# Optimization experiments

Measured on AMD Instinct MI355X. Metric: run time of the kernel, lower is better.

Reference implementation:

```python
import jax, jax.numpy as jnp
import numpy as np

N_HEAD = 4
N_FEAT = 256
D_K = N_FEAT // N_HEAD


def setup_inputs() -> dict:
    key = jax.random.key(0)
    ks = jax.random.split(key, 7)
    B, T, F = 8, 2048, N_FEAT
    return {
        "query": jax.random.normal(ks[0], (B, T, F), dtype=jnp.float32),
        "key": jax.random.normal(ks[1], (B, T, F), dtype=jnp.float32),
        "value": jax.random.normal(ks[2], (B, T, F), dtype=jnp.float32),
        "mask": jax.random.randint(ks[3], (B, 1, T), 0, 2, dtype=jnp.int32),
        "W_qkv": jax.random.normal(ks[4], (3 * F, 3 * F), dtype=jnp.float32) * 0.02,
        "b_qkv": jnp.zeros((3 * F,), dtype=jnp.float32),
        "W_out": jax.random.normal(ks[5], (F, F), dtype=jnp.float32) * 0.02,
        "b_out": jnp.zeros((F,), dtype=jnp.float32),
    }


def reference(query, key, value, mask, W_qkv, b_qkv, W_out, b_out):
    B, T, F = query.shape
    H, dk = N_HEAD, D_K
    # fused QKV projection on concatenated [q; k; v]  -> (B, T, 3F)
    qkv = jnp.concatenate([query, key, value], axis=-1) @ W_qkv.T + b_qkv
    qkv = qkv.reshape(B, T, H, 3 * dk)
    q, k, v = jnp.split(qkv, 3, axis=-1)          # each (B, T, H, dk)
    q = q.transpose(0, 2, 1, 3)                    # (B, H, T, dk)
    k = k.transpose(0, 2, 1, 3)
    v = v.transpose(0, 2, 1, 3)
    scores = jnp.einsum("bhqd,bhkd->bhqk", q, k) / jnp.sqrt(jnp.float32(dk))
    # mask: (B, 1, T) -> broadcast (B, 1, 1, T); positions where mask==0 are masked
    m = (mask[:, None, :, :] == 0)
    min_val = jnp.finfo(scores.dtype).min
    scores = jnp.where(m, min_val, scores)
    attn = jax.nn.softmax(scores, axis=-1)
    attn = jnp.where(m, jnp.float32(0.0), attn)    # zero masked probs, as in torch code
    x = jnp.einsum("bhqk,bhkd->bhqd", attn, v)     # (B, H, T, dk)
    x = x.transpose(0, 2, 1, 3).reshape(B, T, H * dk)
    return x @ W_out.T + b_out
```

## Files before the change

### kernel.cpp

```cpp
#include <hip/hip_runtime.h>
#include <hip/hip_bf16.h>

#define NB 8
#define NT 2048
#define NH 4
#define NF 256
#define NTF 768
#define NM (NB * NT)

typedef unsigned short u16;
typedef unsigned long long u64;
typedef u16 u16x8 __attribute__((ext_vector_type(8)));
typedef __bf16 bf16x8 __attribute__((ext_vector_type(8)));
typedef float f32x4 __attribute__((ext_vector_type(4)));

__device__ __forceinline__ u16 bf16_rne(float f) {
    union { float f; unsigned u; } x; x.f = f;
    unsigned u = x.u;
    return (u16)((u + 0x7fffu + ((u >> 16) & 1u)) >> 16);
}

__device__ __forceinline__ int swz(int row, int colB) {
    return row * 128 + (colB ^ ((row & 7) << 4));
}

__device__ __forceinline__ void glds16(const void* g, void* l) {
    __builtin_amdgcn_global_load_lds(
        (const __attribute__((address_space(1))) void*)g,
        (__attribute__((address_space(3))) void*)l, 16, 0, 0);
}
__device__ __forceinline__ void glds4(const void* g, void* l) {
    __builtin_amdgcn_global_load_lds(
        (const __attribute__((address_space(1))) void*)g,
        (__attribute__((address_space(3))) void*)l, 4, 0, 0);
}

__global__ __launch_bounds__(256) void convert_all_kernel(
        const float* __restrict__ q, const float* __restrict__ k,
        const float* __restrict__ v, const float* __restrict__ wqkv,
        const float* __restrict__ wout, const int* __restrict__ mask,
        u16* __restrict__ xcat, u16* __restrict__ wqkvb,
        u16* __restrict__ woutb, float* __restrict__ maskadd) {
    int bid = blockIdx.x;
    if (bid < 6144) {
        int tid = bid * 256 + threadIdx.x;
        int row = tid / 96;
        int c8  = (tid % 96) * 8;
        const float* src; int c;
        if (c8 < NF)            { src = q; c = c8; }
        else if (c8 < 2 * NF)   { src = k; c = c8 - NF; }
        else                    { src = v; c = c8 - 2 * NF; }
        const float4* p = reinterpret_cast<const float4*>(src + (size_t)row * NF + c);
        float4 a = p[0], b = p[1];
        u16x8 o;
        o[0] = bf16_rne(a.x); o[1] = bf16_rne(a.y); o[2] = bf16_rne(a.z); o[3] = bf16_rne(a.w);
        o[4] = bf16_rne(b.x); o[5] = bf16_rne(b.y); o[6] = bf16_rne(b.z); o[7] = bf16_rne(b.w);
        *reinterpret_cast<u16x8*>(xcat + (size_t)row * NTF + c8) = o;
    } else if (bid < 6464) {
        int tid = (bid - 6144) * 256 + threadIdx.x;
        int i8 = tid * 8;
        const float* src; u16* dst; int off;
        if (i8 < NTF * NTF) { src = wqkv; dst = wqkvb; off = i8; }
        else                { src = wout; dst = woutb; off = i8 - NTF * NTF; }
        const float4* p = reinterpret_cast<const float4*>(src + off);
        float4 a = p[0], b = p[1];
        u16x8 o;
        o[0] = bf16_rne(a.x); o[1] = bf16_rne(a.y); o[2] = bf16_rne(a.z); o[3] = bf16_rne(a.w);
        o[4] = bf16_rne(b.x); o[5] = bf16_rne(b.y); o[6] = bf16_rne(b.z); o[7] = bf16_rne(b.w);
        *reinterpret_cast<u16x8*>(dst + off) = o;
    } else {
        int i = (bid - 6464) * 2048 + threadIdx.x * 8;
        int4 m0 = *reinterpret_cast<const int4*>(mask + i);
        int4 m1 = *reinterpret_cast<const int4*>(mask + i + 4);
        float4 f0 = { m0.x ? 0.f : -1e30f, m0.y ? 0.f : -1e30f,
                      m0.z ? 0.f : -1e30f, m0.w ? 0.f : -1e30f };
        float4 f1 = { m1.x ? 0.f : -1e30f, m1.y ? 0.f : -1e30f,
                      m1.z ? 0.f : -1e30f, m1.w ? 0.f : -1e30f };
        *reinterpret_cast<float4*>(maskadd + i) = f0;
        *reinterpret_cast<float4*>(maskadd + i + 4) = f1;
    }
}

template<int N, int K, int MODE>
__global__ __launch_bounds__(256) void gemm_kernel(
        const u16* __restrict__ A, const u16* __restrict__ Bw,
        const float* __restrict__ bias, void* __restrict__ Cout,
        u16* __restrict__ Vt) {
    __shared__ alignas(16) char smem[32768];
    char* As = smem;
    char* Bs = smem + 16384;
    int m0 = blockIdx.x * 64, n0 = blockIdx.y * 64;
    int tid = threadIdx.x;
    int w = tid >> 6, lane = tid & 63, l15 = lane & 15, hi = lane >> 4;
    int r0 = tid >> 3, cb0 = (tid & 7) * 16;
    int gcb = cb0 ^ ((r0 & 7) << 4);
    int wo = w * 1024;

    const char* Ac = (const char*)A;
    const char* Bc = (const char*)Bw;
    const char* ga0 = Ac + (size_t)(m0 + r0) * (K * 2) + gcb;
    const char* ga1 = ga0 + (size_t)32 * (K * 2);
    const char* gb0 = Bc + (size_t)(n0 + r0) * (K * 2) + gcb;
    const char* gb1 = gb0 + (size_t)32 * (K * 2);

    glds16(ga0, As + wo); glds16(ga1, As + 4096 + wo);
    glds16(gb0, Bs + wo); glds16(gb1, Bs + 4096 + wo);

    f32x4 acc[4];
#pragma unroll
    for (int ct = 0; ct < 4; ++ct) acc[ct] = (f32x4){0.f, 0.f, 0.f, 0.f};

    constexpr int NKT = K / 64;
    for (int kt = 0; kt < NKT; ++kt) {
        int cur = kt & 1;
        __syncthreads();
        if (kt + 1 < NKT) {
            int off = (kt + 1) * 128;
            char* Ad = As + (cur ^ 1) * 8192;
            char* Bd = Bs + (cur ^ 1) * 8192;
            glds16(ga0 + off, Ad + wo); glds16(ga1 + off, Ad + 4096 + wo);
            glds16(gb0 + off, Bd + wo); glds16(gb1 + off, Bd + 4096 + wo);
        }
        const char* Ax = As + cur * 8192;
        const char* Bx = Bs + cur * 8192;
#pragma unroll
        for (int ks = 0; ks < 2; ++ks) {
            bf16x8 af = *reinterpret_cast<const bf16x8*>(Ax + swz(w * 16 + l15, hi * 16 + ks * 64));
#pragma unroll
            for (int ct = 0; ct < 4; ++ct) {
                bf16x8 bf = *reinterpret_cast<const bf16x8*>(Bx + swz(ct * 16 + l15, hi * 16 + ks * 64));
                acc[ct] = __builtin_amdgcn_mfma_f32_16x16x32_bf16(af, bf, acc[ct], 0, 0, 0);
            }
        }
    }

    int orow = m0 + w * 16 + hi * 4;
    if (MODE == 2 && ((n0 >> 6) % 3) == 2) {
        int b = orow >> 11, t = orow & (NT - 1);
        int bh = b * NH + (n0 / 192);
#pragma unroll
        for (int ct = 0; ct < 4; ++ct) {
            int d = ct * 16 + l15;
            float bv = bias[n0 + d];
            union { u16 h4[4]; u64 u; } pk;
#pragma unroll
            for (int r = 0; r < 4; ++r) pk.h4[r] = bf16_rne(acc[ct][r] + bv);
            *reinterpret_cast<u64*>(Vt + (size_t)(bh * 64 + d) * NT + t) = pk.u;
        }
    } else {
#pragma unroll
        for (int ct = 0; ct < 4; ++ct) {
            int col = n0 + ct * 16 + l15;
            float bv = bias[col];
#pragma unroll
            for (int r = 0; r < 4; ++r) {
                float val = acc[ct][r] + bv;
                if (MODE == 1)
                    reinterpret_cast<float*>(Cout)[(size_t)(orow + r) * N + col] = val;
                else
                    reinterpret_cast<u16*>(Cout)[(size_t)(orow + r) * N + col] = bf16_rne(val);
            }
        }
    }
}

__global__ __launch_bounds__(512) void attn_kernel(
        const u16* __restrict__ qkv, const u16* __restrict__ vt,
        const float* __restrict__ maskadd, u16* __restrict__ xout) {
    int bh = blockIdx.x;
    int q0 = blockIdx.y * 128;
    int b = bh >> 2, h = bh & 3;
    __shared__ alignas(16) char smem[49664];
    char* Ps = smem + 32768;
    int tid = threadIdx.x;
    int w = tid >> 6, lane = tid & 63, l15 = lane & 15, hi = lane >> 4;
    int r0 = tid >> 3, cb0 = (tid & 7) * 16;
    int gcb = cb0 ^ ((r0 & 7) << 4);
    int wo = w * 1024;
    const float SCALE = 0.125f * 1.44269504088896340736f;

    const char* qkvC = (const char*)qkv;
    const char* vtC  = (const char*)vt;
    const char* gq0 = qkvC + (size_t)(b * NT + q0 + r0) * 1536 + h * 384 + gcb;
    const char* gq1 = gq0 + (size_t)64 * 1536;
    const char* gk0 = qkvC + (size_t)(b * NT + r0) * 1536 + h * 384 + 128 + gcb;
    const char* gv0 = vtC + (size_t)(bh * 64 + r0) * (NT * 2) + gcb;
    const char* gm  = (const char*)maskadd + (size_t)(b * NT + lane) * 4;

    glds16(gq0, Ps + wo);           glds16(gq1, Ps + 8192 + wo);
    glds16(gk0, smem + wo);
    glds16(gv0, smem + 16384 + wo);
    if (w == 0) glds4(gm, smem + 49152);

    f32x4 accO[4];
#pragma unroll
    for (int ct = 0; ct < 4; ++ct) accO[ct] = (f32x4){0.f, 0.f, 0.f, 0.f};
    float ssum = 0.f;
    bf16x8 bQ[2];
    char* Pw = Ps + w * 2048;

    for (int kt = 0; kt < NT / 64; ++kt) {
        int cur = kt & 1;
        __syncthreads();
        if (kt == 0) {
#pragma unroll
            for (int ks = 0; ks < 2; ++ks)
                bQ[ks] = *reinterpret_cast<const bf16x8*>(Ps + swz(w * 16 + l15, hi * 16 + ks * 64));
        }
        if (kt < NT / 64 - 1) {
            char* Kd = smem + (cur ^ 1) * 8192;
            char* Vd = smem + 16384 + (cur ^ 1) * 8192;
            glds16(gk0 + (size_t)(kt + 1) * 98304, Kd + wo);
            glds16(gv0 + (kt + 1) * 128, Vd + wo);
            if (w == 0) glds4(gm + (kt + 1) * 256, smem + 49152 + (cur ^ 1) * 256);
        }
        const char* Kx = smem + cur * 8192;
        const char* Vx = smem + 16384 + cur * 8192;
        const float* mF = reinterpret_cast<const float*>(smem + 49152 + cur * 256);

        f32x4 s[4];
#pragma unroll
        for (int ct = 0; ct < 4; ++ct) s[ct] = (f32x4){0.f, 0.f, 0.f, 0.f};
        __builtin_amdgcn_s_setprio(1);
#pragma unroll
        for (int ks = 0; ks < 2; ++ks) {
#pragma unroll
            for (int ct = 0; ct < 4; ++ct) {
                bf16x8 aK = *reinterpret_cast<const bf16x8*>(Kx + swz(ct * 16 + l15, hi * 16 + ks * 64));
                s[ct] = __builtin_amdgcn_mfma_f32_16x16x32_bf16(aK, bQ[ks], s[ct], 0, 0, 0);
            }
        }
        __builtin_amdgcn_s_setprio(0);
        float rs = 0.f;
#pragma unroll
        for (int ct = 0; ct < 4; ++ct) {
            f32x4 madd = *reinterpret_cast<const f32x4*>(mF + ct * 16 + hi * 4);
#pragma unroll
            for (int r = 0; r < 4; ++r) {
                float p = exp2f(__builtin_fmaf(s[ct][r], SCALE, madd[r]));
                s[ct][r] = p;
                rs += p;
            }
        }
        ssum += rs;
#pragma unroll
        for (int ct = 0; ct < 4; ++ct) {
            union { __bf16 h4[4]; u64 u; } pk;
#pragma unroll
            for (int r = 0; r < 4; ++r) pk.h4[r] = (__bf16)s[ct][r];
            *reinterpret_cast<u64*>(Pw + swz(l15, ct * 32 + hi * 8)) = pk.u;
        }
        bf16x8 aP[2];
#pragma unroll
        for (int ks = 0; ks < 2; ++ks)
            aP[ks] = *reinterpret_cast<const bf16x8*>(Pw + swz(l15, hi * 16 + ks * 64));
        __builtin_amdgcn_s_setprio(1);
#pragma unroll
        for (int ks = 0; ks < 2; ++ks)
#pragma unroll
            for (int ct = 0; ct < 4; ++ct) {
                bf16x8 bV = *reinterpret_cast<const bf16x8*>(Vx + swz(ct * 16 + l15, hi * 16 + ks * 64));
                accO[ct] = __builtin_amdgcn_mfma_f32_16x16x32_bf16(aP[ks], bV, accO[ct], 0, 0, 0);
            }
        __builtin_amdgcn_s_setprio(0);
    }
    ssum += __shfl_xor(ssum, 16, 64);
    ssum += __shfl_xor(ssum, 32, 64);
    __syncthreads();
    float* sS = reinterpret_cast<float*>(smem + 49152);
    if (hi == 0) sS[w * 16 + l15] = ssum;
    f32x4 sq = *reinterpret_cast<const f32x4*>(sS + w * 16 + hi * 4);
    int qrow = q0 + w * 16 + hi * 4;
#pragma unroll
    for (int r = 0; r < 4; ++r) {
        float inv = sq[r] > 0.f ? 1.0f / sq[r] : 0.0f;
#pragma unroll
        for (int ct = 0; ct < 4; ++ct) {
            int d = ct * 16 + l15;
            xout[(size_t)(b * NT + qrow + r) * NF + h * 64 + d] = bf16_rne(accO[ct][r] * inv);
        }
    }
}

extern "C" void kernel_launch(void* const* d_in, const int* in_sizes, int n_in,
                              void* d_out, int out_size, void* d_ws, size_t ws_size,
                              hipStream_t stream) {
    const float* q    = (const float*)d_in[0];
    const float* k    = (const float*)d_in[1];
    const float* v    = (const float*)d_in[2];
    const int*   mask = (const int*)d_in[3];
    const float* wqkv = (const float*)d_in[4];
    const float* bqkv = (const float*)d_in[5];
    const float* wout = (const float*)d_in[6];
    const float* bout = (const float*)d_in[7];
    float* out = (float*)d_out;

    char* ws = (char*)d_ws;
    u16*   Xcat    = (u16*)(ws);
    u16*   QKV     = (u16*)(ws + 25165824);
    u16*   Vt      = (u16*)(ws + 50331648);
    u16*   Xattn   = (u16*)(ws + 58720256);
    u16*   Wqkvb   = (u16*)(ws + 67108864);
    u16*   Woutb   = (u16*)(ws + 68288512);
    float* Maskadd = (float*)(ws + 68419584);

    convert_all_kernel<<<6472, 256, 0, stream>>>(q, k, v, wqkv, wout, mask,
                                                 Xcat, Wqkvb, Woutb, Maskadd);
    gemm_kernel<NTF, NTF, 2><<<dim3(NM / 64, NTF / 64), 256, 0, stream>>>(
        Xcat, Wqkvb, bqkv, QKV, Vt);
    attn_kernel<<<dim3(NB * NH, NT / 128), 512, 0, stream>>>(QKV, Vt, Maskadd, Xattn);
    gemm_kernel<NF, NF, 1><<<dim3(NM / 64, NF / 64), 256, 0, stream>>>(
        Xattn, Woutb, bout, out, nullptr);
}
```

Baseline: 115.9 us.

## Software-pipeline attention loop: defer PV MFMA by one tile, read mask from global

Restructures the attention inner loop so that the P·V multiply for tile kt-1 runs after the QK^T and softmax of tile kt, with double-buffered P in LDS. V loads are issued one iteration later than K loads so they have a full iteration to land. The mask is now read straight from global memory instead of being staged in LDS. The aim is to overlap exp work with MFMA and drop LDS traffic, at the cost of 64KB of LDS per block, which may lower occupancy.

```diff
diff --git a/kernel.cpp b/kernel.cpp
--- a/kernel.cpp
+++ b/kernel.cpp
@@ -28,11 +28,6 @@
     __builtin_amdgcn_global_load_lds(
         (const __attribute__((address_space(1))) void*)g,
         (__attribute__((address_space(3))) void*)l, 16, 0, 0);
-}
-__device__ __forceinline__ void glds4(const void* g, void* l) {
-    __builtin_amdgcn_global_load_lds(
-        (const __attribute__((address_space(1))) void*)g,
-        (__attribute__((address_space(3))) void*)l, 4, 0, 0);
 }
 
 __global__ __launch_bounds__(256) void convert_all_kernel(
@@ -170,8 +165,10 @@
     int bh = blockIdx.x;
     int q0 = blockIdx.y * 128;
     int b = bh >> 2, h = bh & 3;
-    __shared__ alignas(16) char smem[49664];
-    char* Ps = smem + 32768;
+    __shared__ alignas(16) char smem[65536];
+    char* Kb = smem;
+    char* Vb = smem + 16384;
+    char* Pb = smem + 32768;
     int tid = threadIdx.x;
     int w = tid >> 6, lane = tid & 63, l15 = lane & 15, hi = lane >> 4;
     int r0 = tid >> 3, cb0 = (tid & 7) * 16;
@@ -185,19 +182,17 @@
     const char* gq1 = gq0 + (size_t)64 * 1536;
     const char* gk0 = qkvC + (size_t)(b * NT + r0) * 1536 + h * 384 + 128 + gcb;
     const char* gv0 = vtC + (size_t)(bh * 64 + r0) * (NT * 2) + gcb;
-    const char* gm  = (const char*)maskadd + (size_t)(b * NT + lane) * 4;
-
-    glds16(gq0, Ps + wo);           glds16(gq1, Ps + 8192 + wo);
-    glds16(gk0, smem + wo);
-    glds16(gv0, smem + 16384 + wo);
-    if (w == 0) glds4(gm, smem + 49152);
+    const float* gm = maskadd + (size_t)b * NT;
+
+    glds16(gq0, Pb + 16384 + wo);
+    glds16(gq1, Pb + 16384 + 8192 + wo);
+    glds16(gk0, Kb + wo);
 
     f32x4 accO[4];
 #pragma unroll
     for (int ct = 0; ct < 4; ++ct) accO[ct] = (f32x4){0.f, 0.f, 0.f, 0.f};
     float ssum = 0.f;
     bf16x8 bQ[2];
-    char* Pw = Ps + w * 2048;
 
     for (int kt = 0; kt < NT / 64; ++kt) {
         int cur = kt & 1;
@@ -205,19 +200,14 @@
         if (kt == 0) {
 #pragma unroll
             for (int ks = 0; ks < 2; ++ks)
-                bQ[ks] = *reinterpret_cast<const bf16x8*>(Ps + swz(w * 16 + l15, hi * 16 + ks * 64));
-        }
-        if (kt < NT / 64 - 1) {
-            char* Kd = smem + (cur ^ 1) * 8192;
-            char* Vd = smem + 16384 + (cur ^ 1) * 8192;
-            glds16(gk0 + (size_t)(kt + 1) * 98304, Kd + wo);
-            glds16(gv0 + (kt + 1) * 128, Vd + wo);
-            if (w == 0) glds4(gm + (kt + 1) * 256, smem + 49152 + (cur ^ 1) * 256);
-        }
-        const char* Kx = smem + cur * 8192;
-        const char* Vx = smem + 16384 + cur * 8192;
-        const float* mF = reinterpret_cast<const float*>(smem + 49152 + cur * 256);
-
+                bQ[ks] = *reinterpret_cast<const bf16x8*>(
+                    Pb + 16384 + swz(w * 16 + l15, hi * 16 + ks * 64));
+        }
+        if (kt < NT / 64 - 1)
+            glds16(gk0 + (size_t)(kt + 1) * 98304, Kb + (cur ^ 1) * 8192 + wo);
+        glds16(gv0 + kt * 128, Vb + cur * 8192 + wo);
+
+        const char* Kx = Kb + cur * 8192;
         f32x4 s[4];
 #pragma unroll
         for (int ct = 0; ct < 4; ++ct) s[ct] = (f32x4){0.f, 0.f, 0.f, 0.f};
@@ -231,18 +221,22 @@
             }
         }
         __builtin_amdgcn_s_setprio(0);
+
+        const float4* mrow = reinterpret_cast<const float4*>(gm + kt * 64);
         float rs = 0.f;
 #pragma unroll
         for (int ct = 0; ct < 4; ++ct) {
-            f32x4 madd = *reinterpret_cast<const f32x4*>(mF + ct * 16 + hi * 4);
+            float4 madd = mrow[ct * 4 + hi];
+            float m4[4] = {madd.x, madd.y, madd.z, madd.w};
 #pragma unroll
             for (int r = 0; r < 4; ++r) {
-                float p = exp2f(__builtin_fmaf(s[ct][r], SCALE, madd[r]));
+                float p = exp2f(__builtin_fmaf(s[ct][r], SCALE, m4[r]));
                 s[ct][r] = p;
                 rs += p;
             }
         }
         ssum += rs;
+        char* Pw = Pb + cur * 16384 + w * 2048;
 #pragma unroll
         for (int ct = 0; ct < 4; ++ct) {
             union { __bf16 h4[4]; u64 u; } pk;
@@ -250,11 +244,34 @@
             for (int r = 0; r < 4; ++r) pk.h4[r] = (__bf16)s[ct][r];
             *reinterpret_cast<u64*>(Pw + swz(l15, ct * 32 + hi * 8)) = pk.u;
         }
+
+        if (kt > 0) {
+            char* Pprev = Pb + (cur ^ 1) * 16384 + w * 2048;
+            const char* Vx = Vb + (cur ^ 1) * 8192;
+            bf16x8 aP[2];
+#pragma unroll
+            for (int ks = 0; ks < 2; ++ks)
+                aP[ks] = *reinterpret_cast<const bf16x8*>(Pprev + swz(l15, hi * 16 + ks * 64));
+            __builtin_amdgcn_s_setprio(1);
+#pragma unroll
+            for (int ks = 0; ks < 2; ++ks)
+#pragma unroll
+                for (int ct = 0; ct < 4; ++ct) {
+                    bf16x8 bV = *reinterpret_cast<const bf16x8*>(Vx + swz(ct * 16 + l15, hi * 16 + ks * 64));
+                    accO[ct] = __builtin_amdgcn_mfma_f32_16x16x32_bf16(aP[ks], bV, accO[ct], 0, 0, 0);
+                }
+            __builtin_amdgcn_s_setprio(0);
+        }
+    }
+
+    __syncthreads();
+    {
+        char* Pprev = Pb + 16384 + w * 2048;
+        const char* Vx = Vb + 8192;
         bf16x8 aP[2];
 #pragma unroll
         for (int ks = 0; ks < 2; ++ks)
-            aP[ks] = *reinterpret_cast<const bf16x8*>(Pw + swz(l15, hi * 16 + ks * 64));
-        __builtin_amdgcn_s_setprio(1);
+            aP[ks] = *reinterpret_cast<const bf16x8*>(Pprev + swz(l15, hi * 16 + ks * 64));
 #pragma unroll
         for (int ks = 0; ks < 2; ++ks)
 #pragma unroll
@@ -262,14 +279,12 @@
                 bf16x8 bV = *reinterpret_cast<const bf16x8*>(Vx + swz(ct * 16 + l15, hi * 16 + ks * 64));
                 accO[ct] = __builtin_amdgcn_mfma_f32_16x16x32_bf16(aP[ks], bV, accO[ct], 0, 0, 0);
             }
-        __builtin_amdgcn_s_setprio(0);
     }
     ssum += __shfl_xor(ssum, 16, 64);
     ssum += __shfl_xor(ssum, 32, 64);
-    __syncthreads();
-    float* sS = reinterpret_cast<float*>(smem + 49152);
-    if (hi == 0) sS[w * 16 + l15] = ssum;
-    f32x4 sq = *reinterpret_cast<const f32x4*>(sS + w * 16 + hi * 4);
+    float* sS = reinterpret_cast<float*>(Pb) + w * 16;
+    if (hi == 0) sS[l15] = ssum;
+    f32x4 sq = *reinterpret_cast<const f32x4*>(sS + hi * 4);
     int qrow = q0 + w * 16 + hi * 4;
 #pragma unroll
     for (int r = 0; r < 4; ++r) {
```

Measured after the change: 115.7 us. No clear change (-0.2%).

## Rewrite attention with 32x32 MFMA, register-resident P and split-K warp groups

Applied to the files above, without the earlier changes.

Rewrites the attention kernel to use 32x32x16 bf16 MFMA tiles. Q is held in registers, loaded straight from global, and P is fed to the PV MFMA through v_permlane32_swap instead of a round trip through LDS. The key range is split between two groups of four waves, which are then reduced through LDS at the end. The mask is read directly from global instead of staged in LDS, and two K/V tiles are loaded per iteration. This aims to cut LDS traffic and the number of MFMA instructions, but adds a final cross-group reduction and raises register pressure under the 512,4 launch bound.

```diff
diff --git a/kernel.cpp b/kernel.cpp
--- a/kernel.cpp
+++ b/kernel.cpp
@@ -9,10 +9,12 @@
 #define NM (NB * NT)
 
 typedef unsigned short u16;
+typedef unsigned int u32;
 typedef unsigned long long u64;
 typedef u16 u16x8 __attribute__((ext_vector_type(8)));
 typedef __bf16 bf16x8 __attribute__((ext_vector_type(8)));
 typedef float f32x4 __attribute__((ext_vector_type(4)));
+typedef float f32x16 __attribute__((ext_vector_type(16)));
 
 __device__ __forceinline__ u16 bf16_rne(float f) {
     union { float f; unsigned u; } x; x.f = f;
@@ -29,11 +31,18 @@
         (const __attribute__((address_space(1))) void*)g,
         (__attribute__((address_space(3))) void*)l, 16, 0, 0);
 }
-__device__ __forceinline__ void glds4(const void* g, void* l) {
-    __builtin_amdgcn_global_load_lds(
-        (const __attribute__((address_space(1))) void*)g,
-        (__attribute__((address_space(3))) void*)l, 4, 0, 0);
-}
+
+__device__ __forceinline__ u32 pkbf16(float lo, float hi) {
+    union { __bf16 h2[2]; u32 u; } t;
+    t.h2[0] = (__bf16)lo; t.h2[1] = (__bf16)hi;
+    return t.u;
+}
+
+__device__ __forceinline__ void pl32swap(u32& a, u32& b) {
+    asm("v_permlane32_swap_b32 %0, %1" : "+v"(a), "+v"(b));
+}
+
+#define mfma32(A, B, C) __builtin_amdgcn_mfma_f32_32x32x16_bf16((A), (B), (C), 0, 0, 0)
 
 __global__ __launch_bounds__(256) void convert_all_kernel(
         const float* __restrict__ q, const float* __restrict__ k,
@@ -164,16 +173,17 @@
     }
 }
 
-__global__ __launch_bounds__(512) void attn_kernel(
+__global__ __launch_bounds__(512, 4) void attn_kernel(
         const u16* __restrict__ qkv, const u16* __restrict__ vt,
         const float* __restrict__ maskadd, u16* __restrict__ xout) {
     int bh = blockIdx.x;
     int q0 = blockIdx.y * 128;
     int b = bh >> 2, h = bh & 3;
-    __shared__ alignas(16) char smem[49664];
-    char* Ps = smem + 32768;
+    __shared__ alignas(16) char smem[65536];
     int tid = threadIdx.x;
-    int w = tid >> 6, lane = tid & 63, l15 = lane & 15, hi = lane >> 4;
+    int w = tid >> 6, lane = tid & 63;
+    int l31 = lane & 31, hv = lane >> 5;
+    int wq = w & 3, g = w >> 2;
     int r0 = tid >> 3, cb0 = (tid & 7) * 16;
     int gcb = cb0 ^ ((r0 & 7) << 4);
     int wo = w * 1024;
@@ -181,103 +191,134 @@
 
     const char* qkvC = (const char*)qkv;
     const char* vtC  = (const char*)vt;
-    const char* gq0 = qkvC + (size_t)(b * NT + q0 + r0) * 1536 + h * 384 + gcb;
-    const char* gq1 = gq0 + (size_t)64 * 1536;
     const char* gk0 = qkvC + (size_t)(b * NT + r0) * 1536 + h * 384 + 128 + gcb;
     const char* gv0 = vtC + (size_t)(bh * 64 + r0) * (NT * 2) + gcb;
-    const char* gm  = (const char*)maskadd + (size_t)(b * NT + lane) * 4;
-
-    glds16(gq0, Ps + wo);           glds16(gq1, Ps + 8192 + wo);
-    glds16(gk0, smem + wo);
-    glds16(gv0, smem + 16384 + wo);
-    if (w == 0) glds4(gm, smem + 49152);
-
-    f32x4 accO[4];
-#pragma unroll
-    for (int ct = 0; ct < 4; ++ct) accO[ct] = (f32x4){0.f, 0.f, 0.f, 0.f};
+
+    glds16(gk0,         smem + wo);
+    glds16(gk0 + 98304, smem + 8192 + wo);
+    glds16(gv0,         smem + 32768 + wo);
+    glds16(gv0 + 128,   smem + 32768 + 8192 + wo);
+
+    const char* qrow = qkvC + (size_t)(b * NT + q0 + wq * 32 + l31) * 1536
+                       + h * 384 + hv * 16;
+    bf16x8 bQ0 = *reinterpret_cast<const bf16x8*>(qrow);
+    bf16x8 bQ1 = *reinterpret_cast<const bf16x8*>(qrow + 32);
+    bf16x8 bQ2 = *reinterpret_cast<const bf16x8*>(qrow + 64);
+    bf16x8 bQ3 = *reinterpret_cast<const bf16x8*>(qrow + 96);
+
+    f32x16 accO0 = 0.f, accO1 = 0.f;
     float ssum = 0.f;
-    bf16x8 bQ[2];
-    char* Pw = Ps + w * 2048;
-
-    for (int kt = 0; kt < NT / 64; ++kt) {
-        int cur = kt & 1;
+    const float* gm = maskadd + (size_t)b * NT;
+
+    for (int j = 0; j < 16; ++j) {
+        int cur = j & 1;
         __syncthreads();
-        if (kt == 0) {
-#pragma unroll
-            for (int ks = 0; ks < 2; ++ks)
-                bQ[ks] = *reinterpret_cast<const bf16x8*>(Ps + swz(w * 16 + l15, hi * 16 + ks * 64));
-        }
-        if (kt < NT / 64 - 1) {
-            char* Kd = smem + (cur ^ 1) * 8192;
-            char* Vd = smem + 16384 + (cur ^ 1) * 8192;
-            glds16(gk0 + (size_t)(kt + 1) * 98304, Kd + wo);
-            glds16(gv0 + (kt + 1) * 128, Vd + wo);
-            if (w == 0) glds4(gm + (kt + 1) * 256, smem + 49152 + (cur ^ 1) * 256);
-        }
-        const char* Kx = smem + cur * 8192;
-        const char* Vx = smem + 16384 + cur * 8192;
-        const float* mF = reinterpret_cast<const float*>(smem + 49152 + cur * 256);
-
-        f32x4 s[4];
-#pragma unroll
-        for (int ct = 0; ct < 4; ++ct) s[ct] = (f32x4){0.f, 0.f, 0.f, 0.f};
+        if (j < 15) {
+            int tn = 2 * (j + 1);
+            char* Kd = smem + (cur ^ 1) * 16384;
+            char* Vd = smem + 32768 + (cur ^ 1) * 16384;
+            glds16(gk0 + (size_t)tn * 98304, Kd + wo);
+            glds16(gk0 + (size_t)(tn + 1) * 98304, Kd + 8192 + wo);
+            glds16(gv0 + (size_t)tn * 128, Vd + wo);
+            glds16(gv0 + (size_t)(tn + 1) * 128, Vd + 8192 + wo);
+        }
+        int t = 2 * j + g;
+        const char* Kx = smem + g * 8192 + cur * 16384;
+        const char* Vx = smem + 32768 + g * 8192 + cur * 16384;
+
+        f32x16 s0 = 0.f, s1 = 0.f;
         __builtin_amdgcn_s_setprio(1);
 #pragma unroll
-        for (int ks = 0; ks < 2; ++ks) {
-#pragma unroll
-            for (int ct = 0; ct < 4; ++ct) {
-                bf16x8 aK = *reinterpret_cast<const bf16x8*>(Kx + swz(ct * 16 + l15, hi * 16 + ks * 64));
-                s[ct] = __builtin_amdgcn_mfma_f32_16x16x32_bf16(aK, bQ[ks], s[ct], 0, 0, 0);
+        for (int ks = 0; ks < 4; ++ks) {
+            bf16x8 a0 = *reinterpret_cast<const bf16x8*>(Kx + swz(l31, ks * 32 + hv * 16));
+            bf16x8 a1 = *reinterpret_cast<const bf16x8*>(Kx + swz(32 + l31, ks * 32 + hv * 16));
+            bf16x8 bq = (ks == 0) ? bQ0 : (ks == 1) ? bQ1 : (ks == 2) ? bQ2 : bQ3;
+            s0 = mfma32(a0, bq, s0);
+            s1 = mfma32(a1, bq, s1);
+        }
+        __builtin_amdgcn_s_setprio(0);
+
+        const float* mt = gm + t * 64;
+#pragma unroll
+        for (int rq = 0; rq < 4; ++rq) {
+            f32x4 md0 = *reinterpret_cast<const f32x4*>(mt + rq * 8 + 4 * hv);
+            f32x4 md1 = *reinterpret_cast<const f32x4*>(mt + 32 + rq * 8 + 4 * hv);
+#pragma unroll
+            for (int e = 0; e < 4; ++e) {
+                s0[rq * 4 + e] = __builtin_amdgcn_exp2f(
+                    __builtin_fmaf(s0[rq * 4 + e], SCALE, md0[e]));
+                s1[rq * 4 + e] = __builtin_amdgcn_exp2f(
+                    __builtin_fmaf(s1[rq * 4 + e], SCALE, md1[e]));
             }
         }
+        {
+            f32x16 rv = s0 + s1;
+            union { f32x16 v; f32x4 q[4]; } u; u.v = rv;
+            f32x4 r4 = (u.q[0] + u.q[1]) + (u.q[2] + u.q[3]);
+            ssum += (r4[0] + r4[1]) + (r4[2] + r4[3]);
+        }
+
+        u32 pka0[4], pkb0[4], pka1[4], pkb1[4];
+#pragma unroll
+        for (int rq = 0; rq < 4; ++rq) {
+            pka0[rq] = pkbf16(s0[rq * 4 + 0], s0[rq * 4 + 1]);
+            pkb0[rq] = pkbf16(s0[rq * 4 + 2], s0[rq * 4 + 3]);
+            pka1[rq] = pkbf16(s1[rq * 4 + 0], s1[rq * 4 + 1]);
+            pkb1[rq] = pkbf16(s1[rq * 4 + 2], s1[rq * 4 + 3]);
+        }
+        __builtin_amdgcn_s_setprio(1);
+#pragma unroll
+        for (int s4 = 0; s4 < 4; ++s4) {
+            const int kb = s4 >> 1, sp = (s4 & 1) * 2;
+            u32 B0, B1, B2, B3;
+            if (kb == 0) { B0 = pka0[sp]; B2 = pka0[sp + 1]; B1 = pkb0[sp]; B3 = pkb0[sp + 1]; }
+            else         { B0 = pka1[sp]; B2 = pka1[sp + 1]; B1 = pkb1[sp]; B3 = pkb1[sp + 1]; }
+            pl32swap(B0, B2);
+            pl32swap(B1, B3);
+            union { u32 u4[4]; bf16x8 v; } bp;
+            bp.u4[0] = B0; bp.u4[1] = B1; bp.u4[2] = B2; bp.u4[3] = B3;
+            bf16x8 av0 = *reinterpret_cast<const bf16x8*>(Vx + swz(l31, s4 * 32 + hv * 16));
+            bf16x8 av1 = *reinterpret_cast<const bf16x8*>(Vx + swz(32 + l31, s4 * 32 + hv * 16));
+            accO0 = mfma32(av0, bp.v, accO0);
+            accO1 = mfma32(av1, bp.v, accO1);
+        }
         __builtin_amdgcn_s_setprio(0);
-        float rs = 0.f;
-#pragma unroll
-        for (int ct = 0; ct < 4; ++ct) {
-            f32x4 madd = *reinterpret_cast<const f32x4*>(mF + ct * 16 + hi * 4);
-#pragma unroll
-            for (int r = 0; r < 4; ++r) {
-                float p = exp2f(__builtin_fmaf(s[ct][r], SCALE, madd[r]));
-                s[ct][r] = p;
-                rs += p;
-            }
-        }
-        ssum += rs;
-#pragma unroll
-        for (int ct = 0; ct < 4; ++ct) {
-            union { __bf16 h4[4]; u64 u; } pk;
-#pragma unroll
-            for (int r = 0; r < 4; ++r) pk.h4[r] = (__bf16)s[ct][r];
-            *reinterpret_cast<u64*>(Pw + swz(l15, ct * 32 + hi * 8)) = pk.u;
-        }
-        bf16x8 aP[2];
-#pragma unroll
-        for (int ks = 0; ks < 2; ++ks)
-            aP[ks] = *reinterpret_cast<const bf16x8*>(Pw + swz(l15, hi * 16 + ks * 64));
-        __builtin_amdgcn_s_setprio(1);
-#pragma unroll
-        for (int ks = 0; ks < 2; ++ks)
-#pragma unroll
-            for (int ct = 0; ct < 4; ++ct) {
-                bf16x8 bV = *reinterpret_cast<const bf16x8*>(Vx + swz(ct * 16 + l15, hi * 16 + ks * 64));
-                accO[ct] = __builtin_amdgcn_mfma_f32_16x16x32_bf16(aP[ks], bV, accO[ct], 0, 0, 0);
-            }
-        __builtin_amdgcn_s_setprio(0);
-    }
-    ssum += __shfl_xor(ssum, 16, 64);
+    }
+
     ssum += __shfl_xor(ssum, 32, 64);
     __syncthreads();
-    float* sS = reinterpret_cast<float*>(smem + 49152);
-    if (hi == 0) sS[w * 16 + l15] = ssum;
-    f32x4 sq = *reinterpret_cast<const f32x4*>(sS + w * 16 + hi * 4);
-    int qrow = q0 + w * 16 + hi * 4;
-#pragma unroll
-    for (int r = 0; r < 4; ++r) {
-        float inv = sq[r] > 0.f ? 1.0f / sq[r] : 0.0f;
-#pragma unroll
-        for (int ct = 0; ct < 4; ++ct) {
-            int d = ct * 16 + l15;
-            xout[(size_t)(b * NT + qrow + r) * NF + h * 64 + d] = bf16_rne(accO[ct][r] * inv);
+    float* sS = reinterpret_cast<float*>(smem + 32768);
+    if (g == 1) {
+        union { f32x16 v; f32x4 q[4]; } o0, o1; o0.v = accO0; o1.v = accO1;
+#pragma unroll
+        for (int i = 0; i < 4; ++i) {
+            *reinterpret_cast<f32x4*>(smem + wq * 8192 + i * 1024 + lane * 16) = o0.q[i];
+            *reinterpret_cast<f32x4*>(smem + wq * 8192 + (4 + i) * 1024 + lane * 16) = o1.q[i];
+        }
+        if (lane < 32) sS[wq * 32 + l31] = ssum;
+    }
+    __syncthreads();
+    if (g == 0) {
+        union { f32x16 v; f32x4 q[4]; } o0, o1; o0.v = accO0; o1.v = accO1;
+#pragma unroll
+        for (int i = 0; i < 4; ++i) {
+            o0.q[i] += *reinterpret_cast<const f32x4*>(smem + wq * 8192 + i * 1024 + lane * 16);
+            o1.q[i] += *reinterpret_cast<const f32x4*>(smem + wq * 8192 + (4 + i) * 1024 + lane * 16);
+        }
+        float stot = ssum + sS[wq * 32 + l31];
+        float inv = stot > 0.f ? 1.0f / stot : 0.0f;
+        int qg = b * NT + q0 + wq * 32 + l31;
+#pragma unroll
+        for (int db = 0; db < 2; ++db) {
+            const float* of = db ? (const float*)&o1.v : (const float*)&o0.v;
+#pragma unroll
+            for (int rq = 0; rq < 4; ++rq) {
+                u32 lo = pkbf16(of[rq * 4 + 0] * inv, of[rq * 4 + 1] * inv);
+                u32 hi2 = pkbf16(of[rq * 4 + 2] * inv, of[rq * 4 + 3] * inv);
+                u64 pk = (u64)lo | ((u64)hi2 << 32);
+                int d = db * 32 + rq * 8 + 4 * hv;
+                *reinterpret_cast<u64*>(xout + (size_t)qg * NF + h * 64 + d) = pk;
+            }
         }
     }
 }
```

Result: faster. 104.4 us (-10.0%).
